# Performance work log

Hardware: AMD Instinct MI355X
Metric: run time of the kernel (lower is better)

The kernel has to match this reference:

```python
import jax, jax.numpy as jnp
import numpy as np

BITS = 4
GROUP = 128
IN = 4096
OUT = 14336
B = 64
PACK = 32 // BITS          # 8 values per int32
MAXQ = (1 << BITS) - 1     # 15


def setup_inputs() -> dict:
    key = jax.random.key(0)
    k = jax.random.split(key, 5)
    x = jax.random.normal(k[0], (B, IN), dtype=jnp.float32)
    # non-negative int32 so arithmetic right-shift behaves like logical shift
    qweight = jax.random.randint(k[1], (IN // PACK, OUT), 0, 2**31 - 1, dtype=jnp.int32)
    qzeros = jax.random.randint(k[2], (IN // GROUP, OUT // PACK), 0, 2**31 - 1, dtype=jnp.int32)
    scales = jax.random.uniform(k[3], (IN // GROUP, OUT), dtype=jnp.float32,
                                minval=1e-3, maxval=1e-2)
    bias = jax.random.normal(k[4], (OUT,), dtype=jnp.float32) * 0.01
    g_idx = (jnp.arange(IN) // GROUP).astype(jnp.int32)
    return dict(x=x, qweight=qweight, qzeros=qzeros, scales=scales, bias=bias, g_idx=g_idx)


def _dequant(qweight, qzeros, scales, g_idx):
    shifts = jnp.arange(PACK, dtype=jnp.int32) * BITS  # [PACK]
    # unpack weights: [IN//PACK, PACK, OUT] -> [IN, OUT]
    w = (qweight[:, None, :] >> shifts[None, :, None]) & MAXQ
    w = w.reshape(IN, OUT)
    # unpack zeros: [G, OUT//PACK, PACK] -> [G, OUT]; pack() stored (zeros-1), so add 1 back
    z = (qzeros[:, :, None] >> shifts[None, None, :]) & MAXQ
    z = z.reshape(-1, OUT) + 1
    # per-group dequant with arbitrary g_idx (act-order support)
    return scales[g_idx] * (w - z[g_idx]).astype(scales.dtype)


def reference(x, qweight, qzeros, scales, bias, g_idx):
    W = _dequant(qweight, qzeros, scales, g_idx)  # [IN, OUT]
    return x @ W + bias
```

## Files before the change

kernel.cpp:

```cpp
#include <hip/hip_runtime.h>
#include <hip/hip_bf16.h>

using u32 = unsigned int;
using u16 = unsigned short;

typedef __attribute__((ext_vector_type(8))) _Float16 half8;
typedef __attribute__((ext_vector_type(2))) _Float16 half2v;
typedef __attribute__((ext_vector_type(16))) float f32x16;
typedef __attribute__((ext_vector_type(4))) u32 u32x4;

#define IN_K   4096
#define OUT_N  14336
#define NST    16

__global__ __launch_bounds__(256) void prep_kernel(const float* __restrict__ x,
                                                   u16* __restrict__ xs) {
  const int t = blockIdx.x * 256 + threadIdx.x;
  const int c = t >> 6;
  const int r = t & 63;
  const float* px = x + r * IN_K + c * 8;
  const float4 a = *(const float4*)px;
  const float4 b = *(const float4*)(px + 4);
  const float af[4] = {a.x, a.y, a.z, a.w};
  const float bf[4] = {b.x, b.y, b.z, b.w};
  union { u32x4 v; u32 u[4]; } o;
#pragma unroll
  for (int i = 0; i < 4; ++i) {
    const _Float16 hl = (_Float16)af[i];
    const _Float16 hh = (_Float16)bf[i];
    u16 lo, hi;
    __builtin_memcpy(&lo, &hl, 2);
    __builtin_memcpy(&hi, &hh, 2);
    o.u[i] = (u32)lo | ((u32)hi << 16);
  }
  *(u32x4*)(xs + (size_t)t * 8) = o.v;
}

static __device__ __forceinline__ half8 dequant8(u32 q, half2v hz, half2v s2) {
  const u32 p0 = (q & 0x000F000Fu) | 0x64006400u;
  const u32 p1 = ((q >> 4) & 0x000F000Fu) | 0x64006400u;
  const u32 p2 = ((q >> 8) & 0x000F000Fu) | 0x64006400u;
  const u32 p3 = ((q >> 12) & 0x000F000Fu) | 0x64006400u;
  half2v t0, t1, t2, t3;
  __builtin_memcpy(&t0, &p0, 4);
  __builtin_memcpy(&t1, &p1, 4);
  __builtin_memcpy(&t2, &p2, 4);
  __builtin_memcpy(&t3, &p3, 4);
  union { half8 v; half2v h[4]; } bb;
  bb.h[0] = (t0 - hz) * s2;
  bb.h[1] = (t1 - hz) * s2;
  bb.h[2] = (t2 - hz) * s2;
  bb.h[3] = (t3 - hz) * s2;
  return bb.v;
}

__global__ __launch_bounds__(256, 2) void qgemm_kernel(
    const u32* __restrict__ qw, const u32* __restrict__ qz,
    const float* __restrict__ scal, const u16* __restrict__ xs,
    const float* __restrict__ bias, float* __restrict__ out) {
  __shared__ alignas(16) char smem[73728];
  const int tid = threadIdx.x;
  const int lane = tid & 63;
  const int g = lane >> 5;
  const int nn = lane & 31;
  const int kq = tid >> 6;
  const int bx = blockIdx.x;
  const int bxp = (bx & 7) * 56 + (bx >> 3);
  const int colabs = bxp * 32 + nn;
  const int zsh = (nn & 7) * 4;
  char* const base = smem + kq * 18432;

  f32x16 acc0, acc1;
#pragma unroll
  for (int i = 0; i < 16; ++i) { acc0[i] = 0.f; acc1[i] = 0.f; }

  float sv[8]; u32 zv[8];
#pragma unroll
  for (int t = 0; t < 8; ++t) {
    sv[t] = scal[(size_t)(kq * 8 + t) * OUT_N + colabs];
    zv[t] = qz[(size_t)(kq * 8 + t) * (OUT_N / 8) + (colabs >> 3)];
  }
  asm volatile("s_waitcnt vmcnt(0)" ::: "memory");

  auto issue = [&](int st) {
    const int slot = st & 1;
    char* ab = base + slot * 8192;
    char* qb = base + 16384 + slot * 1024;
    const u16* asrc = xs + (size_t)(kq * 128 + st * 8) * 512;
#pragma unroll
    for (int r = 0; r < 8; ++r) {
      const int p = r * 64 + lane;
      __builtin_amdgcn_global_load_lds(
          (const __attribute__((address_space(1))) void*)(asrc + p * 8),
          (__attribute__((address_space(3))) void*)(ab + p * 16), 16, 0, 0);
    }
    const int j = lane >> 3, cg = lane & 7;
    const u32* qsrc = qw + (size_t)(kq * 128 + st * 8 + j) * OUT_N
                         + bxp * 32 + cg * 4;
    __builtin_amdgcn_global_load_lds(
        (const __attribute__((address_space(1))) void*)qsrc,
        (__attribute__((address_space(3))) void*)(qb + lane * 16), 16, 0, 0);
  };

  issue(0); issue(1);

#pragma unroll
  for (int st = 0; st < NST; ++st) {
    if (st < NST - 1)
      asm volatile("s_waitcnt vmcnt(9)" ::: "memory");
    else
      asm volatile("s_waitcnt vmcnt(0)" ::: "memory");

    const int gi = st >> 1;
    const u32 zq = (zv[gi] >> zsh) & 0xFu;
    const u32 hzu = 0x64016401u + zq * 0x00010001u;
    half2v hz; __builtin_memcpy(&hz, &hzu, 4);
    const _Float16 hs = (_Float16)sv[gi];
    const half2v s2 = {hs, hs};

    const u16* ab = (const u16*)(base + (st & 1) * 8192);
    const u32* qb = (const u32*)(base + 16384 + (st & 1) * 1024);
    __builtin_amdgcn_s_setprio(1);
#pragma unroll
    for (int s = 0; s < 4; ++s) {
      const int cl = s * 2 + g;
      const half8 a0 = *(const half8*)(ab + (cl * 64 + nn) * 8);
      const half8 a1 = *(const half8*)(ab + (cl * 64 + nn + 32) * 8);
      const u32 q = qb[cl * 32 + nn];
      const half8 bb = dequant8(q, hz, s2);
      acc0 = __builtin_amdgcn_mfma_f32_32x32x16_f16(a0, bb, acc0, 0, 0, 0);
      acc1 = __builtin_amdgcn_mfma_f32_32x32x16_f16(a1, bb, acc1, 0, 0, 0);
    }
    __builtin_amdgcn_s_setprio(0);

    if (st + 2 < NST) {
      asm volatile("s_waitcnt lgkmcnt(0)" ::: "memory");
      issue(st + 2);
    }
  }

  __syncthreads();
  float* ep = (float*)smem + kq * 2048;
#pragma unroll
  for (int r = 0; r < 16; ++r) {
    const int row0 = (r & 3) + 8 * (r >> 2) + 4 * g;
    ep[row0 * 32 + nn] = acc0[r];
    ep[(row0 + 32) * 32 + nn] = acc1[r];
  }
  __syncthreads();
  const int pos = tid * 8;
  const int row = pos >> 5;
  const int colb = pos & 31;
  const float* eb = (const float*)smem;
  float4 v0 = *(const float4*)(bias + bxp * 32 + colb);
  float4 v1 = *(const float4*)(bias + bxp * 32 + colb + 4);
#pragma unroll
  for (int q = 0; q < 4; ++q) {
    const float4 a = *(const float4*)(eb + q * 2048 + pos);
    const float4 b = *(const float4*)(eb + q * 2048 + pos + 4);
    v0.x += a.x; v0.y += a.y; v0.z += a.z; v0.w += a.w;
    v1.x += b.x; v1.y += b.y; v1.z += b.z; v1.w += b.w;
  }
  float* po = out + (size_t)row * OUT_N + bxp * 32 + colb;
  *(float4*)po = v0;
  *(float4*)(po + 4) = v1;
}

extern "C" void kernel_launch(void* const* d_in, const int* in_sizes, int n_in,
                              void* d_out, int out_size, void* d_ws, size_t ws_size,
                              hipStream_t stream) {
  (void)in_sizes; (void)n_in; (void)out_size; (void)ws_size;
  const float* x    = (const float*)d_in[0];
  const u32*   qw   = (const u32*)d_in[1];
  const u32*   qz   = (const u32*)d_in[2];
  const float* sc   = (const float*)d_in[3];
  const float* bias = (const float*)d_in[4];
  float* out = (float*)d_out;
  u16* xs = (u16*)d_ws;

  prep_kernel<<<128, 256, 0, stream>>>(x, xs);
  qgemm_kernel<<<448, 256, 0, stream>>>(qw, qz, sc, xs, bias, out);
}
```

Measured before the change: 26.74 us.

## Deepen qweight prefetch to eight stages with triple-buffered activations

```diff
diff --git a/kernel.cpp b/kernel.cpp
--- a/kernel.cpp
+++ b/kernel.cpp
@@ -11,7 +11,7 @@
 
 #define IN_K   4096
 #define OUT_N  14336
-#define NST    16
+#define NST    32
 
 __global__ __launch_bounds__(256) void prep_kernel(const float* __restrict__ x,
                                                    u16* __restrict__ xs) {
@@ -58,7 +58,7 @@
     const u32* __restrict__ qw, const u32* __restrict__ qz,
     const float* __restrict__ scal, const u16* __restrict__ xs,
     const float* __restrict__ bias, float* __restrict__ out) {
-  __shared__ alignas(16) char smem[73728];
+  __shared__ alignas(16) char smem[65536];
   const int tid = threadIdx.x;
   const int lane = tid & 63;
   const int g = lane >> 5;
@@ -68,7 +68,7 @@
   const int bxp = (bx & 7) * 56 + (bx >> 3);
   const int colabs = bxp * 32 + nn;
   const int zsh = (nn & 7) * 4;
-  char* const base = smem + kq * 18432;
+  char* const base = smem + kq * 16384;
 
   f32x16 acc0, acc1;
 #pragma unroll
@@ -82,61 +82,71 @@
   }
   asm volatile("s_waitcnt vmcnt(0)" ::: "memory");
 
-  auto issue = [&](int st) {
-    const int slot = st & 1;
-    char* ab = base + slot * 8192;
-    char* qb = base + 16384 + slot * 1024;
-    const u16* asrc = xs + (size_t)(kq * 128 + st * 8) * 512;
+  auto issueA = [&](int st) {
+    char* ab = base + (st % 3) * 4096;
+    const u16* asrc = xs + (size_t)(kq * 128 + st * 4) * 512;
 #pragma unroll
-    for (int r = 0; r < 8; ++r) {
+    for (int r = 0; r < 4; ++r) {
       const int p = r * 64 + lane;
       __builtin_amdgcn_global_load_lds(
           (const __attribute__((address_space(1))) void*)(asrc + p * 8),
           (__attribute__((address_space(3))) void*)(ab + p * 16), 16, 0, 0);
     }
-    const int j = lane >> 3, cg = lane & 7;
-    const u32* qsrc = qw + (size_t)(kq * 128 + st * 8 + j) * OUT_N
-                         + bxp * 32 + cg * 4;
-    __builtin_amdgcn_global_load_lds(
-        (const __attribute__((address_space(1))) void*)qsrc,
-        (__attribute__((address_space(3))) void*)(qb + lane * 16), 16, 0, 0);
+  };
+  auto issueQ = [&](int st) {
+    char* qb = base + 12288 + (st & 7) * 512;
+#pragma unroll
+    for (int r = 0; r < 2; ++r) {
+      const int row = kq * 128 + st * 4 + 2 * r + (lane >> 5);
+      const u32* src = qw + (size_t)row * OUT_N + bxp * 32 + (lane & 31);
+      __builtin_amdgcn_global_load_lds(
+          (const __attribute__((address_space(1))) void*)src,
+          (__attribute__((address_space(3))) void*)(qb + r * 256 + lane * 4),
+          4, 0, 0);
+    }
   };
 
-  issue(0); issue(1);
+  issueA(0); issueA(1); issueA(2);
+#pragma unroll
+  for (int i = 0; i < 8; ++i) issueQ(i);
 
 #pragma unroll
   for (int st = 0; st < NST; ++st) {
-    if (st < NST - 1)
-      asm volatile("s_waitcnt vmcnt(9)" ::: "memory");
-    else
-      asm volatile("s_waitcnt vmcnt(0)" ::: "memory");
+    if (st == 0)       asm volatile("s_waitcnt vmcnt(14)" ::: "memory");
+    else if (st == 1)  asm volatile("s_waitcnt vmcnt(18)" ::: "memory");
+    else if (st == 2)  asm volatile("s_waitcnt vmcnt(22)" ::: "memory");
+    else if (st <= 24) asm volatile("s_waitcnt vmcnt(14)" ::: "memory");
+    else if (st == 25) asm volatile("s_waitcnt vmcnt(12)" ::: "memory");
+    else if (st == 26) asm volatile("s_waitcnt vmcnt(10)" ::: "memory");
+    else if (st <= 29) asm volatile("s_waitcnt vmcnt(8)" ::: "memory");
+    else if (st == 30) asm volatile("s_waitcnt vmcnt(4)" ::: "memory");
+    else               asm volatile("s_waitcnt vmcnt(0)" ::: "memory");
 
-    const int gi = st >> 1;
+    const int gi = st >> 2;
     const u32 zq = (zv[gi] >> zsh) & 0xFu;
     const u32 hzu = 0x64016401u + zq * 0x00010001u;
     half2v hz; __builtin_memcpy(&hz, &hzu, 4);
     const _Float16 hs = (_Float16)sv[gi];
     const half2v s2 = {hs, hs};
 
-    const u16* ab = (const u16*)(base + (st & 1) * 8192);
-    const u32* qb = (const u32*)(base + 16384 + (st & 1) * 1024);
+    const char* ab = base + (st % 3) * 4096;
+    const char* qb = base + 12288 + (st & 7) * 512;
     __builtin_amdgcn_s_setprio(1);
 #pragma unroll
-    for (int s = 0; s < 4; ++s) {
+    for (int s = 0; s < 2; ++s) {
       const int cl = s * 2 + g;
-      const half8 a0 = *(const half8*)(ab + (cl * 64 + nn) * 8);
-      const half8 a1 = *(const half8*)(ab + (cl * 64 + nn + 32) * 8);
-      const u32 q = qb[cl * 32 + nn];
+      const half8 a0 = *(const half8*)(ab + (cl * 64 + nn) * 16);
+      const half8 a1 = *(const half8*)(ab + (cl * 64 + nn + 32) * 16);
+      const u32 q = *(const u32*)(qb + (cl * 32 + nn) * 4);
       const half8 bb = dequant8(q, hz, s2);
       acc0 = __builtin_amdgcn_mfma_f32_32x32x16_f16(a0, bb, acc0, 0, 0, 0);
       acc1 = __builtin_amdgcn_mfma_f32_32x32x16_f16(a1, bb, acc1, 0, 0, 0);
     }
     __builtin_amdgcn_s_setprio(0);
 
-    if (st + 2 < NST) {
-      asm volatile("s_waitcnt lgkmcnt(0)" ::: "memory");
-      issue(st + 2);
-    }
+    asm volatile("s_waitcnt lgkmcnt(0)" ::: "memory");
+    if (st + 3 < NST) issueA(st + 3);
+    if (st + 8 < NST) issueQ(st + 8);
   }
 
   __syncthreads();
```

Measured after the change: 26.43 us. Within noise of the previous version (-1.2%).

## Repack quantized weights into tile-contiguous layout before GEMM

Applied to the files above, without the earlier changes.

```diff
diff --git a/kernel.cpp b/kernel.cpp
--- a/kernel.cpp
+++ b/kernel.cpp
@@ -34,6 +34,30 @@
     o.u[i] = (u32)lo | ((u32)hi << 16);
   }
   *(u32x4*)(xs + (size_t)t * 8) = o.v;
+}
+
+__global__ __launch_bounds__(256) void repack_kernel(const u32* __restrict__ qw,
+                                                     u32* __restrict__ qwt) {
+  __shared__ u32 lds[32][257];
+  const int wg = blockIdx.x;
+  const int rt = wg / 56, ct = wg % 56;
+  const int row0 = rt * 32;
+  const int col0 = ct * 256;
+  const int t = threadIdx.x;
+#pragma unroll
+  for (int r = 0; r < 32; ++r)
+    lds[r][t] = qw[(size_t)(row0 + r) * OUT_N + col0 + t];
+  __syncthreads();
+  const int row = t >> 3, cg = t & 7;
+#pragma unroll
+  for (int cb = 0; cb < 8; ++cb) {
+    const u32 a0 = lds[row][cb * 32 + cg * 4 + 0];
+    const u32 a1 = lds[row][cb * 32 + cg * 4 + 1];
+    const u32 a2 = lds[row][cb * 32 + cg * 4 + 2];
+    const u32 a3 = lds[row][cb * 32 + cg * 4 + 3];
+    u32x4 v = {a0, a1, a2, a3};
+    *(u32x4*)(qwt + ((size_t)(ct * 8 + cb) * 512 + row0 + row) * 32 + cg * 4) = v;
+  }
 }
 
 static __device__ __forceinline__ half8 dequant8(u32 q, half2v hz, half2v s2) {
@@ -54,8 +78,9 @@
   return bb.v;
 }
 
+template <bool SEQQ>
 __global__ __launch_bounds__(256, 2) void qgemm_kernel(
-    const u32* __restrict__ qw, const u32* __restrict__ qz,
+    const u32* __restrict__ qwsrc, const u32* __restrict__ qz,
     const float* __restrict__ scal, const u16* __restrict__ xs,
     const float* __restrict__ bias, float* __restrict__ out) {
   __shared__ alignas(16) char smem[73728];
@@ -82,6 +107,8 @@
   }
   asm volatile("s_waitcnt vmcnt(0)" ::: "memory");
 
+  const u32* qseq = qwsrc + ((size_t)bxp * 512 + kq * 128) * 32;
+
   auto issue = [&](int st) {
     const int slot = st & 1;
     char* ab = base + slot * 8192;
@@ -94,12 +121,18 @@
           (const __attribute__((address_space(1))) void*)(asrc + p * 8),
           (__attribute__((address_space(3))) void*)(ab + p * 16), 16, 0, 0);
     }
-    const int j = lane >> 3, cg = lane & 7;
-    const u32* qsrc = qw + (size_t)(kq * 128 + st * 8 + j) * OUT_N
-                         + bxp * 32 + cg * 4;
-    __builtin_amdgcn_global_load_lds(
-        (const __attribute__((address_space(1))) void*)qsrc,
-        (__attribute__((address_space(3))) void*)(qb + lane * 16), 16, 0, 0);
+    if (SEQQ) {
+      __builtin_amdgcn_global_load_lds(
+          (const __attribute__((address_space(1))) void*)(qseq + st * 256 + lane * 4),
+          (__attribute__((address_space(3))) void*)(qb + lane * 16), 16, 0, 0);
+    } else {
+      const int j = lane >> 3, cg = lane & 7;
+      const u32* src = qwsrc + (size_t)(kq * 128 + st * 8 + j) * OUT_N
+                             + bxp * 32 + cg * 4;
+      __builtin_amdgcn_global_load_lds(
+          (const __attribute__((address_space(1))) void*)src,
+          (__attribute__((address_space(3))) void*)(qb + lane * 16), 16, 0, 0);
+    }
   };
 
   issue(0); issue(1);
@@ -169,15 +202,25 @@
 extern "C" void kernel_launch(void* const* d_in, const int* in_sizes, int n_in,
                               void* d_out, int out_size, void* d_ws, size_t ws_size,
                               hipStream_t stream) {
-  (void)in_sizes; (void)n_in; (void)out_size; (void)ws_size;
+  (void)in_sizes; (void)n_in; (void)out_size;
   const float* x    = (const float*)d_in[0];
   const u32*   qw   = (const u32*)d_in[1];
   const u32*   qz   = (const u32*)d_in[2];
   const float* sc   = (const float*)d_in[3];
   const float* bias = (const float*)d_in[4];
   float* out = (float*)d_out;
+
+  const size_t XS_BYTES  = (size_t)64 * IN_K * 2;
+  const size_t QWT_BYTES = (size_t)448 * 512 * 32 * 4;
   u16* xs = (u16*)d_ws;
 
   prep_kernel<<<128, 256, 0, stream>>>(x, xs);
-  qgemm_kernel<<<448, 256, 0, stream>>>(qw, qz, sc, xs, bias, out);
-}
+
+  if (ws_size >= XS_BYTES + QWT_BYTES) {
+    u32* qwt = (u32*)((char*)d_ws + XS_BYTES);
+    repack_kernel<<<896, 256, 0, stream>>>(qw, qwt);
+    qgemm_kernel<true><<<448, 256, 0, stream>>>(qwt, qz, sc, xs, bias, out);
+  } else {
+    qgemm_kernel<false><<<448, 256, 0, stream>>>(qw, qz, sc, xs, bias, out);
+  }
+}
```

Measured after the change: 36.62 us. +36.9%, slower.
